# Kernel optimization log

Hardware: AMD Instinct MI355X
Metric: run time of the kernel (lower is better)

The kernel has to match this reference:

```python
import math
import jax, jax.numpy as jnp
import numpy as np

B, T, C = 2, 2048, 1024
HEADS = 16
HD = C // HEADS  # 64


def setup_inputs() -> dict:
    key = jax.random.key(0)
    ks = jax.random.split(key, 5)
    s = 0.02
    return {
        "x": jax.random.normal(ks[0], (B, T, C), jnp.float32),
        "Wq": jax.random.normal(ks[1], (C, C), jnp.float32) * s,
        "bq": jnp.zeros((C,), jnp.float32),
        "Wk": jax.random.normal(ks[2], (C, HD), jnp.float32) * s,
        "bk": jnp.zeros((HD,), jnp.float32),
        "Wv": jax.random.normal(ks[3], (C, HD), jnp.float32) * s,
        "bv": jnp.zeros((HD,), jnp.float32),
        "Wo": jax.random.normal(ks[4], (C, C), jnp.float32) * s,
        "bo": jnp.zeros((C,), jnp.float32),
    }


def _rope_tables(seq_len, dim):
    pos = jnp.arange(seq_len, dtype=jnp.float32)
    freqs = 1.0 / (10000.0 ** (jnp.arange(0, dim, 2, dtype=jnp.float32) / dim))
    ang = pos[:, None] * freqs[None, :]          # (T, dim//2)
    # broadcast over (B, T, H, dim//2)
    return jnp.sin(ang)[None, :, None, :], jnp.cos(ang)[None, :, None, :]


def _apply_rope(t, sin, cos, dim):
    t1, t2 = t[..., : dim // 2], t[..., dim // 2 :]
    # matches torch source: emb[..., :d/2]=sin, emb[..., d/2:]=cos
    return jnp.concatenate([t1 * cos + t2 * sin, t1 * sin - t2 * cos], axis=-1)


def reference(x, Wq, bq, Wk, bk, Wv, bv, Wo, bo):
    Bx, Tx, Cx = x.shape
    q = (x @ Wq + bq).reshape(Bx, Tx, HEADS, HD)   # (B,T,H,hd)
    k = (x @ Wk + bk)[:, :, None, :]               # (B,T,1,hd) single KV head (MQA)
    v = (x @ Wv + bv)[:, :, None, :]
    sin, cos = _rope_tables(Tx, HD)
    q = _apply_rope(q, sin, cos, HD)
    k = _apply_rope(k, sin, cos, HD)
    att = jnp.einsum('bthd,bThd->bhtT', q, k) / math.sqrt(HD)
    causal = jnp.triu(jnp.ones((Tx, Tx), bool), 1)
    att = jnp.where(causal, -jnp.inf, att)
    att = jax.nn.softmax(att, axis=-1)
    out = jnp.einsum('bhtT,bThd->bthd', att, v).reshape(Bx, Tx, Cx)
    return out @ Wo + bo
```

## Files before the change

kernel.cpp:

```cpp
#include <hip/hip_runtime.h>
#include <math.h>

#define BSZ   2
#define TSEQ  2048
#define CDIM  1024
#define NHEAD 16
#define HDIM  64
#define BT    (BSZ*TSEQ)
#define NQKV  1152

typedef __attribute__((ext_vector_type(8))) short short8;
typedef __attribute__((ext_vector_type(4))) float f32x4;
typedef unsigned short u16;
typedef unsigned int   u32;

__device__ __forceinline__ u16 f2b(float f) {
    union { float f; u32 u; } c; c.f = f;
    u32 u = c.u;
    u += 0x7fffu + ((u >> 16) & 1u);
    return (u16)(u >> 16);
}
__device__ __forceinline__ u32 pack2(float lo, float hi) {
    return (u32)f2b(lo) | ((u32)f2b(hi) << 16);
}

__device__ __forceinline__ void async_copy16(const void* g, void* l) {
    __builtin_amdgcn_global_load_lds(
        (__attribute__((address_space(1))) const void*)g,
        (__attribute__((address_space(3))) void*)l,
        16, 0, 0);
}

__device__ __forceinline__ void transpose_tile(
    const float* __restrict__ W, u16* __restrict__ Wt,
    int K, int Nw, int nofs, int bx, int by, float (*T)[65])
{
    const int tid = threadIdx.x;
    const int k0 = by * 64, n0 = bx * 64;
    #pragma unroll
    for (int i = 0; i < 16; ++i) {
        int idx = i * 256 + tid, r = idx >> 6, c = idx & 63;
        T[r][c] = W[(size_t)(k0 + r) * Nw + n0 + c];
    }
    __syncthreads();
    #pragma unroll
    for (int i = 0; i < 16; ++i) {
        int idx = i * 256 + tid, rn = idx >> 6, ck = idx & 63;
        Wt[(size_t)(nofs + n0 + rn) * K + k0 + ck] = f2b(T[ck][rn]);
    }
}

__global__ __launch_bounds__(256) void prep_kernel(
    const float* __restrict__ x,
    const float* __restrict__ Wq, const float* __restrict__ Wk,
    const float* __restrict__ Wv, const float* __restrict__ Wo,
    const float* __restrict__ bq, const float* __restrict__ bk,
    const float* __restrict__ bv,
    u16* __restrict__ xb,
    u16* __restrict__ Wqkvt, u16* __restrict__ Wot, float* __restrict__ bqkv)
{
    __shared__ float T[64][65];
    const int bid = blockIdx.x;
    if (bid < 4096) {
        int i = bid * 256 + threadIdx.x;
        float4 f = ((const float4*)x)[i];
        u16* d = xb + (size_t)i * 4;
        d[0] = f2b(f.x); d[1] = f2b(f.y); d[2] = f2b(f.z); d[3] = f2b(f.w);
    } else if (bid < 4352) {
        int b2 = bid - 4096;
        transpose_tile(Wq, Wqkvt, 1024, 1024, 0, b2 & 15, b2 >> 4, T);
    } else if (bid < 4368) {
        transpose_tile(Wk, Wqkvt, 1024, 64, 1024, 0, bid - 4352, T);
    } else if (bid < 4384) {
        transpose_tile(Wv, Wqkvt, 1024, 64, 1088, 0, bid - 4368, T);
    } else if (bid < 4640) {
        int b2 = bid - 4384;
        transpose_tile(Wo, Wot, 1024, 1024, 0, b2 & 15, b2 >> 4, T);
    } else {
        for (int i = threadIdx.x; i < NQKV; i += 256)
            bqkv[i] = (i < 1024) ? bq[i] : (i < 1088 ? bk[i - 1024] : bv[i - 1088]);
    }
}

__device__ __forceinline__ void gemm_step(
    const u16* __restrict__ As, const u16* __restrict__ Bs,
    int wm, int wn, int quad, int ln16, f32x4 (*acc)[4])
{
    short8 af[2], bf[4];
    #pragma unroll
    for (int mt = 0; mt < 2; ++mt)
        af[mt] = *(const short8*)&As[(((wm * 2 + mt) * 64) + quad * 16 + ln16) * 8];
    #pragma unroll
    for (int nt = 0; nt < 4; ++nt)
        bf[nt] = *(const short8*)&Bs[(((wn * 4 + nt) * 64) + quad * 16 + ln16) * 8];
    #pragma unroll
    for (int mt = 0; mt < 2; ++mt)
        #pragma unroll
        for (int nt = 0; nt < 4; ++nt)
            acc[mt][nt] = __builtin_amdgcn_mfma_f32_16x16x32_bf16(
                af[mt], bf[nt], acc[mt][nt], 0, 0, 0);
}

__global__ __launch_bounds__(256) void gemm_qkv_kernel(
    const u16* __restrict__ A, const u16* __restrict__ Bt,
    const float* __restrict__ bias,
    u16* __restrict__ qb, u16* __restrict__ kb, u16* __restrict__ vT)
{
    __shared__ __align__(16) u16 AsC[2][64 * 32];
    __shared__ __align__(16) u16 BsC[2][128 * 32];
    const int tid  = threadIdx.x;
    const int wave = tid >> 6, lane = tid & 63;
    const int ln16 = lane & 15, quad = lane >> 4;
    const int wm = wave >> 1, wn = wave & 1;
    const int m0 = blockIdx.y * 64, n0 = blockIdx.x * 128;
    const int K = CDIM;

    const int c_row = ((tid >> 6) << 4) + (tid & 15);
    const int c_k   = ((tid >> 4) & 3) * 8;
    const u16* ag  = &A [(size_t)(m0 + c_row)       * K + c_k];
    const u16* bg0 = &Bt[(size_t)(n0 + c_row)       * K + c_k];
    const u16* bg1 = &Bt[(size_t)(n0 + 64 + c_row)  * K + c_k];
    u16* a_l [2] = { &AsC[0][(size_t)wave * 64 * 8],       &AsC[1][(size_t)wave * 64 * 8] };
    u16* b_l0[2] = { &BsC[0][(size_t)wave * 64 * 8],       &BsC[1][(size_t)wave * 64 * 8] };
    u16* b_l1[2] = { &BsC[0][(size_t)(wave + 4) * 64 * 8], &BsC[1][(size_t)(wave + 4) * 64 * 8] };

    f32x4 acc[2][4];
    #pragma unroll
    for (int i = 0; i < 2; ++i)
        #pragma unroll
        for (int j = 0; j < 4; ++j) acc[i][j] = (f32x4){0.f, 0.f, 0.f, 0.f};

    async_copy16(ag, a_l[0]); async_copy16(bg0, b_l0[0]); async_copy16(bg1, b_l1[0]);
    __syncthreads();

    for (int k0 = 0; k0 < K; k0 += 64) {
        async_copy16(ag + 32, a_l[1]);
        async_copy16(bg0 + 32, b_l0[1]);
        async_copy16(bg1 + 32, b_l1[1]);
        gemm_step(AsC[0], BsC[0], wm, wn, quad, ln16, acc);
        __syncthreads();
        if (k0 + 64 < K) {
            async_copy16(ag + 64, a_l[0]);
            async_copy16(bg0 + 64, b_l0[0]);
            async_copy16(bg1 + 64, b_l1[0]);
        }
        gemm_step(AsC[1], BsC[1], wm, wn, quad, ln16, acc);
        __syncthreads();
        ag += 64; bg0 += 64; bg1 += 64;
    }

    #pragma unroll
    for (int mt = 0; mt < 2; ++mt)
        #pragma unroll
        for (int nt = 0; nt < 4; ++nt) {
            float bb = bias[n0 + wn * 64 + nt * 16 + ln16];
            #pragma unroll
            for (int r = 0; r < 4; ++r) acc[mt][nt][r] += bb;
        }

    const int col0 = n0 + wn * 64;
    if (col0 < 1024) {
        const int hh = col0 >> 6;
        #pragma unroll
        for (int nt = 0; nt < 2; ++nt) {
            int j = nt * 16 + ln16;
            float fr = exp2f(-0.41524101186092029f * (float)j);
            #pragma unroll
            for (int mt = 0; mt < 2; ++mt)
                #pragma unroll
                for (int r = 0; r < 4; ++r) {
                    int m = m0 + wm * 32 + mt * 16 + quad * 4 + r;
                    float sn, cs;
                    __sincosf((float)(m & (TSEQ - 1)) * fr, &sn, &cs);
                    float t1 = acc[mt][nt][r], t2 = acc[mt][nt + 2][r];
                    u16* o = qb + (size_t)m * CDIM + hh * 64 + j;
                    o[0]  = f2b(fmaf(t1, cs,  t2 * sn) * 0.18033688011112043f);
                    o[32] = f2b(fmaf(t1, sn, -t2 * cs) * 0.18033688011112043f);
                }
        }
    } else if (wn == 0) {
        #pragma unroll
        for (int nt = 0; nt < 2; ++nt) {
            int j = nt * 16 + ln16;
            float fr = exp2f(-0.41524101186092029f * (float)j);
            #pragma unroll
            for (int mt = 0; mt < 2; ++mt)
                #pragma unroll
                for (int r = 0; r < 4; ++r) {
                    int m = m0 + wm * 32 + mt * 16 + quad * 4 + r;
                    float sn, cs;
                    __sincosf((float)(m & (TSEQ - 1)) * fr, &sn, &cs);
                    float t1 = acc[mt][nt][r], t2 = acc[mt][nt + 2][r];
                    u16* o = kb + (size_t)m * HDIM + j;
                    o[0]  = f2b(fmaf(t1, cs,  t2 * sn));
                    o[32] = f2b(fmaf(t1, sn, -t2 * cs));
                }
        }
    } else {
        #pragma unroll
        for (int nt = 0; nt < 4; ++nt) {
            int d = nt * 16 + ln16;
            #pragma unroll
            for (int mt = 0; mt < 2; ++mt) {
                int mr = m0 + wm * 32 + mt * 16 + quad * 4;
                int b  = mr >> 11, tq = mr & (TSEQ - 1);
                uint2 val;
                val.x = pack2(acc[mt][nt][0], acc[mt][nt][1]);
                val.y = pack2(acc[mt][nt][2], acc[mt][nt][3]);
                *(uint2*)&vT[(size_t)(b * HDIM + d) * TSEQ + tq] = val;
            }
        }
    }
}

__global__ __launch_bounds__(256) void gemm_mfma_kernel(
    const u16* __restrict__ A, const u16* __restrict__ Bt,
    const float* __restrict__ bias, float* __restrict__ Y,
    int M, int N, int K)
{
    __shared__ __align__(16) u16 AsC[2][64 * 32];
    __shared__ __align__(16) u16 BsC[2][128 * 32];
    const int tid  = threadIdx.x;
    const int wave = tid >> 6, lane = tid & 63;
    const int ln16 = lane & 15, quad = lane >> 4;
    const int wm = wave >> 1, wn = wave & 1;
    const int m0 = blockIdx.y * 64, n0 = blockIdx.x * 128;

    const int c_row = ((tid >> 6) << 4) + (tid & 15);
    const int c_k   = ((tid >> 4) & 3) * 8;
    const u16* ag  = &A [(size_t)(m0 + c_row)       * K + c_k];
    const u16* bg0 = &Bt[(size_t)(n0 + c_row)       * K + c_k];
    const u16* bg1 = &Bt[(size_t)(n0 + 64 + c_row)  * K + c_k];
    u16* a_l [2] = { &AsC[0][(size_t)wave * 64 * 8],       &AsC[1][(size_t)wave * 64 * 8] };
    u16* b_l0[2] = { &BsC[0][(size_t)wave * 64 * 8],       &BsC[1][(size_t)wave * 64 * 8] };
    u16* b_l1[2] = { &BsC[0][(size_t)(wave + 4) * 64 * 8], &BsC[1][(size_t)(wave + 4) * 64 * 8] };

    f32x4 acc[2][4];
    #pragma unroll
    for (int i = 0; i < 2; ++i)
        #pragma unroll
        for (int j = 0; j < 4; ++j) acc[i][j] = (f32x4){0.f, 0.f, 0.f, 0.f};

    async_copy16(ag, a_l[0]); async_copy16(bg0, b_l0[0]); async_copy16(bg1, b_l1[0]);
    __syncthreads();

    for (int k0 = 0; k0 < K; k0 += 64) {
        async_copy16(ag + 32, a_l[1]);
        async_copy16(bg0 + 32, b_l0[1]);
        async_copy16(bg1 + 32, b_l1[1]);
        gemm_step(AsC[0], BsC[0], wm, wn, quad, ln16, acc);
        __syncthreads();
        if (k0 + 64 < K) {
            async_copy16(ag + 64, a_l[0]);
            async_copy16(bg0 + 64, b_l0[0]);
            async_copy16(bg1 + 64, b_l1[0]);
        }
        gemm_step(AsC[1], BsC[1], wm, wn, quad, ln16, acc);
        __syncthreads();
        ag += 64; bg0 += 64; bg1 += 64;
    }

    #pragma unroll
    for (int mt = 0; mt < 2; ++mt)
        #pragma unroll
        for (int nt = 0; nt < 4; ++nt) {
            int n = n0 + wn * 64 + nt * 16 + ln16;
            float bb = bias[n];
            #pragma unroll
            for (int r = 0; r < 4; ++r) {
                int m = m0 + wm * 32 + mt * 16 + quad * 4 + r;
                Y[(size_t)m * N + n] = acc[mt][nt][r] + bb;
            }
        }
}

__device__ __forceinline__ void flash_stage_kv(
    const u16* __restrict__ kb, const u16* __restrict__ vT,
    int b, int kt, u16* __restrict__ Ksb, u16* __restrict__ Vsb,
    const int* row_c, const int* off_c, int c0)
{
    const size_t kt0 = (size_t)(b * TSEQ + kt * 64);
    #pragma unroll
    for (int hf = 0; hf < 2; ++hf) {
        int cc = c0 + hf * 256;
        async_copy16(kb + (kt0 + row_c[hf]) * HDIM + off_c[hf], Ksb + cc * 8);
        async_copy16(vT + (size_t)(b * HDIM + row_c[hf]) * TSEQ + kt * 64 + off_c[hf],
                     Vsb + cc * 8);
    }
}

__device__ __forceinline__ void flash_tile(
    const u16* __restrict__ Ksb, const u16* __restrict__ Vsb,
    const u16* __restrict__ Qs, u16* __restrict__ Pw,
    int wave, int ln16, int quad, bool diag,
    f32x4* lacc, f32x4* oacc)
{
    f32x4 sv[4];
    #pragma unroll
    for (int t = 0; t < 4; ++t) sv[t] = (f32x4){0.f, 0.f, 0.f, 0.f};
    #pragma unroll
    for (int kk2 = 0; kk2 < 2; ++kk2) {
        short8 af = *(const short8*)&Qs[(wave * 128 + kk2 * 64 + quad * 16 + ln16) * 8];
        #pragma unroll
        for (int t = 0; t < 4; ++t) {
            short8 bf = *(const short8*)&Ksb[(t * 128 + kk2 * 64 + quad * 16 + ln16) * 8];
            sv[t] = __builtin_amdgcn_mfma_f32_16x16x32_bf16(af, bf, sv[t], 0, 0, 0);
        }
    }

    if (diag) {
        #pragma unroll
        for (int t = 0; t < 4; ++t) {
            int key = t * 16 + ln16;
            #pragma unroll
            for (int r = 0; r < 4; ++r) {
                float e = (key > wave * 16 + quad * 4 + r) ? 0.f : exp2f(sv[t][r]);
                Pw[(quad * 4 + r) * 72 + t * 16 + ln16] =
                    (u16)(__float_as_uint(e) >> 16);
            }
        }
    } else {
        #pragma unroll
        for (int t = 0; t < 4; ++t)
            #pragma unroll
            for (int r = 0; r < 4; ++r) {
                float e = exp2f(sv[t][r]);
                Pw[(quad * 4 + r) * 72 + t * 16 + ln16] =
                    (u16)(__float_as_uint(e) >> 16);
            }
    }

    const short8 ones = {0x3F80, 0x3F80, 0x3F80, 0x3F80,
                         0x3F80, 0x3F80, 0x3F80, 0x3F80};
    #pragma unroll
    for (int kk2 = 0; kk2 < 2; ++kk2) {
        short8 pf = *(const short8*)&Pw[ln16 * 72 + kk2 * 32 + quad * 8];
        *lacc = __builtin_amdgcn_mfma_f32_16x16x32_bf16(pf, ones, *lacc, 0, 0, 0);
        #pragma unroll
        for (int t = 0; t < 4; ++t) {
            short8 vf = *(const short8*)&Vsb[(t * 128 + kk2 * 64 + quad * 16 + ln16) * 8];
            oacc[t] = __builtin_amdgcn_mfma_f32_16x16x32_bf16(pf, vf, oacc[t], 0, 0, 0);
        }
    }
}

__global__ __launch_bounds__(256) void flash_mfma_kernel(
    const u16* __restrict__ qb, const u16* __restrict__ kb,
    const u16* __restrict__ vT, u16* __restrict__ o)
{
    const int id  = blockIdx.x;
    const int qt  = 31 - (id >> 5);
    const int hb  = id & 31;
    const int h   = hb >> 1;
    const int b   = hb & 1;
    __shared__ __align__(16) u16 Qs [512 * 8];
    __shared__ __align__(16) u16 Ks0[512 * 8];
    __shared__ __align__(16) u16 Ks1[512 * 8];
    __shared__ __align__(16) u16 Vs0[512 * 8];
    __shared__ __align__(16) u16 Vs1[512 * 8];
    __shared__ __align__(16) u16 Ps[4 * 16 * 72];

    const int tid  = threadIdx.x;
    const int wave = tid >> 6, lane = tid & 63;
    const int ln16 = lane & 15, quad = lane >> 4;

    const int c0 = tid;
    int row_c[2], off_c[2];
    #pragma unroll
    for (int hf = 0; hf < 2; ++hf) {
        int c = c0 + hf * 256;
        row_c[hf] = ((c >> 7) << 4) | (c & 15);
        off_c[hf] = ((c >> 6) & 1) * 32 + ((c >> 4) & 3) * 8;
    }

    u16* Pw = &Ps[wave * 16 * 72];

    #pragma unroll
    for (int hf = 0; hf < 2; ++hf)
        async_copy16(
            qb + (size_t)(b * TSEQ + qt * 64 + row_c[hf]) * CDIM + h * HDIM + off_c[hf],
            Qs + (c0 + hf * 256) * 8);
    flash_stage_kv(kb, vT, b, 0, Ks0, Vs0, row_c, off_c, c0);

    f32x4 lacc = (f32x4){0.f, 0.f, 0.f, 0.f};
    f32x4 oacc[4];
    #pragma unroll
    for (int t = 0; t < 4; ++t) oacc[t] = (f32x4){0.f, 0.f, 0.f, 0.f};

    int kt = 0;
    while (true) {
        __syncthreads();
        if (kt < qt) flash_stage_kv(kb, vT, b, kt + 1, Ks1, Vs1, row_c, off_c, c0);
        flash_tile(Ks0, Vs0, Qs, Pw, wave, ln16, quad, kt == qt, &lacc, oacc);
        if (++kt > qt) break;
        __syncthreads();
        if (kt < qt) flash_stage_kv(kb, vT, b, kt + 1, Ks0, Vs0, row_c, off_c, c0);
        flash_tile(Ks1, Vs1, Qs, Pw, wave, ln16, quad, kt == qt, &lacc, oacc);
        if (++kt > qt) break;
    }

    float inv[4];
    #pragma unroll
    for (int r = 0; r < 4; ++r) inv[r] = 1.0f / lacc[r];
    #pragma unroll
    for (int t = 0; t < 4; ++t) {
        #pragma unroll
        for (int r = 0; r < 4; ++r) {
            int row = qt * 64 + wave * 16 + quad * 4 + r;
            int d   = t * 16 + ln16;
            o[(size_t)(b * TSEQ + row) * CDIM + h * HDIM + d] = f2b(oacc[t][r] * inv[r]);
        }
    }
}

extern "C" void kernel_launch(void* const* d_in, const int* in_sizes, int n_in,
                              void* d_out, int out_size, void* d_ws, size_t ws_size,
                              hipStream_t stream)
{
    const float* x  = (const float*)d_in[0];
    const float* Wq = (const float*)d_in[1];
    const float* bq = (const float*)d_in[2];
    const float* Wk = (const float*)d_in[3];
    const float* bk = (const float*)d_in[4];
    const float* Wv = (const float*)d_in[5];
    const float* bv = (const float*)d_in[6];
    const float* Wo = (const float*)d_in[7];
    const float* bo = (const float*)d_in[8];
    float* out = (float*)d_out;

    const size_t MB = 1u << 20;
    char* w = (char*)d_ws;
    u16*   xb   = (u16*)(w);
    u16*   aob  = (u16*)(w);
    u16*   qb   = (u16*)(w + 8 * MB);
    u16*   kb   = (u16*)(w + 16 * MB);
    u16*   vT   = (u16*)(w + 16 * MB + 512 * 1024);
    u16*   Wqkvt= (u16*)(w + 17 * MB);
    u16*   Wot  = (u16*)(w + 20 * MB);
    float* bqkv = (float*)(w + 22 * MB);

    prep_kernel<<<dim3(4641), dim3(256), 0, stream>>>(
        x, Wq, Wk, Wv, Wo, bq, bk, bv, xb, Wqkvt, Wot, bqkv);
    gemm_qkv_kernel<<<dim3(NQKV / 128, BT / 64), dim3(256), 0, stream>>>(
        xb, Wqkvt, bqkv, qb, kb, vT);
    flash_mfma_kernel<<<dim3(32 * NHEAD * BSZ), dim3(256), 0, stream>>>(
        qb, kb, vT, aob);
    gemm_mfma_kernel<<<dim3(CDIM / 128, BT / 64), dim3(256), 0, stream>>>(
        aob, Wot, bo, out, BT, CDIM, CDIM);
}
```

Before: 193.6 us.

## Triple-buffer GEMM LDS stages with vmcnt-gated barriers for deeper prefetch

Replaces the double-buffered K loop in both the QKV and output-projection GEMMs with a three-stage LDS ring. Two tiles are prefetched ahead, and each step waits with s_waitcnt vmcnt(3) plus a raw s_barrier rather than a full __syncthreads. The aim is to hide more global-load latency behind MFMA work. It costs 50% more shared memory, which may lower occupancy, and it hardcodes K=1024 (32 k-steps), so a different K would give wrong results.

```diff
diff --git a/kernel.cpp b/kernel.cpp
--- a/kernel.cpp
+++ b/kernel.cpp
@@ -101,13 +101,47 @@
                 af[mt], bf[nt], acc[mt][nt], 0, 0, 0);
 }
 
+__device__ __forceinline__ void gemm_stage(
+    const u16* ag, const u16* bg0, const u16* bg1,
+    u16* al, u16* bl0, u16* bl1)
+{
+    async_copy16(ag,  al);
+    async_copy16(bg0, bl0);
+    async_copy16(bg1, bl1);
+}
+
+#define GEMM_PIPE_LOOP()                                                        \
+    gemm_stage(ag,      bg0,      bg1,      aL0, bL00, bL10);                   \
+    gemm_stage(ag + 32, bg0 + 32, bg1 + 32, aL1, bL01, bL11);                   \
+    for (int k = 0; k < 30; k += 3) {                                           \
+        const u16 *agk = ag + k * 32, *bg0k = bg0 + k * 32, *bg1k = bg1 + k * 32; \
+        asm volatile("s_waitcnt vmcnt(3)" ::: "memory");                        \
+        __builtin_amdgcn_s_barrier();                                           \
+        gemm_stage(agk + 64, bg0k + 64, bg1k + 64, aL2, bL02, bL12);            \
+        gemm_step(AsC[0], BsC[0], wm, wn, quad, ln16, acc);                     \
+        asm volatile("s_waitcnt vmcnt(3)" ::: "memory");                        \
+        __builtin_amdgcn_s_barrier();                                           \
+        gemm_stage(agk + 96, bg0k + 96, bg1k + 96, aL0, bL00, bL10);            \
+        gemm_step(AsC[1], BsC[1], wm, wn, quad, ln16, acc);                     \
+        asm volatile("s_waitcnt vmcnt(3)" ::: "memory");                        \
+        __builtin_amdgcn_s_barrier();                                           \
+        gemm_stage(agk + 128, bg0k + 128, bg1k + 128, aL1, bL01, bL11);         \
+        gemm_step(AsC[2], BsC[2], wm, wn, quad, ln16, acc);                     \
+    }                                                                           \
+    asm volatile("s_waitcnt vmcnt(3)" ::: "memory");                            \
+    __builtin_amdgcn_s_barrier();                                               \
+    gemm_step(AsC[0], BsC[0], wm, wn, quad, ln16, acc);                         \
+    asm volatile("s_waitcnt vmcnt(0)" ::: "memory");                            \
+    __builtin_amdgcn_s_barrier();                                               \
+    gemm_step(AsC[1], BsC[1], wm, wn, quad, ln16, acc);
+
 __global__ __launch_bounds__(256) void gemm_qkv_kernel(
     const u16* __restrict__ A, const u16* __restrict__ Bt,
     const float* __restrict__ bias,
     u16* __restrict__ qb, u16* __restrict__ kb, u16* __restrict__ vT)
 {
-    __shared__ __align__(16) u16 AsC[2][64 * 32];
-    __shared__ __align__(16) u16 BsC[2][128 * 32];
+    __shared__ __align__(16) u16 AsC[3][64 * 32];
+    __shared__ __align__(16) u16 BsC[3][128 * 32];
     const int tid  = threadIdx.x;
     const int wave = tid >> 6, lane = tid & 63;
     const int ln16 = lane & 15, quad = lane >> 4;
@@ -120,9 +154,15 @@
     const u16* ag  = &A [(size_t)(m0 + c_row)       * K + c_k];
     const u16* bg0 = &Bt[(size_t)(n0 + c_row)       * K + c_k];
     const u16* bg1 = &Bt[(size_t)(n0 + 64 + c_row)  * K + c_k];
-    u16* a_l [2] = { &AsC[0][(size_t)wave * 64 * 8],       &AsC[1][(size_t)wave * 64 * 8] };
-    u16* b_l0[2] = { &BsC[0][(size_t)wave * 64 * 8],       &BsC[1][(size_t)wave * 64 * 8] };
-    u16* b_l1[2] = { &BsC[0][(size_t)(wave + 4) * 64 * 8], &BsC[1][(size_t)(wave + 4) * 64 * 8] };
+    u16* aL0  = &AsC[0][(size_t)wave * 512];
+    u16* aL1  = &AsC[1][(size_t)wave * 512];
+    u16* aL2  = &AsC[2][(size_t)wave * 512];
+    u16* bL00 = &BsC[0][(size_t)wave * 512];
+    u16* bL01 = &BsC[1][(size_t)wave * 512];
+    u16* bL02 = &BsC[2][(size_t)wave * 512];
+    u16* bL10 = &BsC[0][(size_t)(wave + 4) * 512];
+    u16* bL11 = &BsC[1][(size_t)(wave + 4) * 512];
+    u16* bL12 = &BsC[2][(size_t)(wave + 4) * 512];
 
     f32x4 acc[2][4];
     #pragma unroll
@@ -130,24 +170,7 @@
         #pragma unroll
         for (int j = 0; j < 4; ++j) acc[i][j] = (f32x4){0.f, 0.f, 0.f, 0.f};
 
-    async_copy16(ag, a_l[0]); async_copy16(bg0, b_l0[0]); async_copy16(bg1, b_l1[0]);
-    __syncthreads();
-
-    for (int k0 = 0; k0 < K; k0 += 64) {
-        async_copy16(ag + 32, a_l[1]);
-        async_copy16(bg0 + 32, b_l0[1]);
-        async_copy16(bg1 + 32, b_l1[1]);
-        gemm_step(AsC[0], BsC[0], wm, wn, quad, ln16, acc);
-        __syncthreads();
-        if (k0 + 64 < K) {
-            async_copy16(ag + 64, a_l[0]);
-            async_copy16(bg0 + 64, b_l0[0]);
-            async_copy16(bg1 + 64, b_l1[0]);
-        }
-        gemm_step(AsC[1], BsC[1], wm, wn, quad, ln16, acc);
-        __syncthreads();
-        ag += 64; bg0 += 64; bg1 += 64;
-    }
+    GEMM_PIPE_LOOP();
 
     #pragma unroll
     for (int mt = 0; mt < 2; ++mt)
@@ -218,8 +241,8 @@
     const float* __restrict__ bias, float* __restrict__ Y,
     int M, int N, int K)
 {
-    __shared__ __align__(16) u16 AsC[2][64 * 32];
-    __shared__ __align__(16) u16 BsC[2][128 * 32];
+    __shared__ __align__(16) u16 AsC[3][64 * 32];
+    __shared__ __align__(16) u16 BsC[3][128 * 32];
     const int tid  = threadIdx.x;
     const int wave = tid >> 6, lane = tid & 63;
     const int ln16 = lane & 15, quad = lane >> 4;
@@ -231,9 +254,15 @@
     const u16* ag  = &A [(size_t)(m0 + c_row)       * K + c_k];
     const u16* bg0 = &Bt[(size_t)(n0 + c_row)       * K + c_k];
     const u16* bg1 = &Bt[(size_t)(n0 + 64 + c_row)  * K + c_k];
-    u16* a_l [2] = { &AsC[0][(size_t)wave * 64 * 8],       &AsC[1][(size_t)wave * 64 * 8] };
-    u16* b_l0[2] = { &BsC[0][(size_t)wave * 64 * 8],       &BsC[1][(size_t)wave * 64 * 8] };
-    u16* b_l1[2] = { &BsC[0][(size_t)(wave + 4) * 64 * 8], &BsC[1][(size_t)(wave + 4) * 64 * 8] };
+    u16* aL0  = &AsC[0][(size_t)wave * 512];
+    u16* aL1  = &AsC[1][(size_t)wave * 512];
+    u16* aL2  = &AsC[2][(size_t)wave * 512];
+    u16* bL00 = &BsC[0][(size_t)wave * 512];
+    u16* bL01 = &BsC[1][(size_t)wave * 512];
+    u16* bL02 = &BsC[2][(size_t)wave * 512];
+    u16* bL10 = &BsC[0][(size_t)(wave + 4) * 512];
+    u16* bL11 = &BsC[1][(size_t)(wave + 4) * 512];
+    u16* bL12 = &BsC[2][(size_t)(wave + 4) * 512];
 
     f32x4 acc[2][4];
     #pragma unroll
@@ -241,24 +270,7 @@
         #pragma unroll
         for (int j = 0; j < 4; ++j) acc[i][j] = (f32x4){0.f, 0.f, 0.f, 0.f};
 
-    async_copy16(ag, a_l[0]); async_copy16(bg0, b_l0[0]); async_copy16(bg1, b_l1[0]);
-    __syncthreads();
-
-    for (int k0 = 0; k0 < K; k0 += 64) {
-        async_copy16(ag + 32, a_l[1]);
-        async_copy16(bg0 + 32, b_l0[1]);
-        async_copy16(bg1 + 32, b_l1[1]);
-        gemm_step(AsC[0], BsC[0], wm, wn, quad, ln16, acc);
-        __syncthreads();
-        if (k0 + 64 < K) {
-            async_copy16(ag + 64, a_l[0]);
-            async_copy16(bg0 + 64, b_l0[0]);
-            async_copy16(bg1 + 64, b_l1[0]);
-        }
-        gemm_step(AsC[1], BsC[1], wm, wn, quad, ln16, acc);
-        __syncthreads();
-        ag += 64; bg0 += 64; bg1 += 64;
-    }
+    GEMM_PIPE_LOOP();
 
     #pragma unroll
     for (int mt = 0; mt < 2; ++mt)
```

After: 192.2 us. About the same (-0.7%).
